# Optimization experiments

Hardware: AMD Instinct MI355X
Metric: run time of the kernel (lower is better)

## Reference

```python
import jax, jax.numpy as jnp
import numpy as np

NUM_HEADS = 16  # matches init_kwargs


def _linear(x, W, b):
    # torch nn.Linear: x @ W.T + b
    return jnp.matmul(x, W.T) + b


def setup_inputs() -> dict:
    key = jax.random.key(0)
    ks = jax.random.split(key, 5)
    B, S, Dm = 8, 2048, 1024
    scale = 0.02
    return {
        "q": jax.random.normal(ks[0], (B, S, Dm), dtype=jnp.float32),
        "k": jax.random.normal(ks[1], (B, S, Dm), dtype=jnp.float32),
        "v": jax.random.normal(ks[2], (B, S, Dm), dtype=jnp.float32),
        "W": jax.random.normal(ks[3], (Dm, Dm), dtype=jnp.float32) * scale,
        "b": jax.random.normal(ks[4], (Dm,), dtype=jnp.float32) * scale,
    }


def reference(q, k, v, W, b):
    B, S, Dm = q.shape
    H = NUM_HEADS
    D = Dm // H  # head_dim

    def proj(x):
        # linear -> view(B, S, H, D) -> transpose(2, 3): (B, S, D, H)
        # NOTE: original code transposes dims 2 and 3 (head_dim <-> heads),
        # NOT the usual (1, 2); we reproduce that exactly.
        y = _linear(x, W, b).reshape(B, S, H, D)
        return jnp.swapaxes(y, 2, 3)  # (B, S, D, H)

    qh, kh, vh = proj(q), proj(k), proj(v)

    # scores: (B, S, D, H) @ (B, S, H, D) -> (B, S, D, D), scaled by sqrt(head_dim)
    logits = jnp.einsum("bsdh,bseh->bsde", qh, kh) / jnp.sqrt(jnp.float32(D))
    attn = jax.nn.softmax(logits, axis=-1)
    out = jnp.einsum("bsde,bseh->bsdh", attn, vh)  # (B, S, D, H)

    # transpose(1, 2) -> (B, D, S, H), then view(B, -1, model_dim)
    concat = jnp.swapaxes(out, 1, 2).reshape(B, -1, Dm)  # (B, S, Dm)
    return _linear(concat, W, b)
```

## Files before the change

kernel.cpp:

```cpp
#include <hip/hip_runtime.h>
#include <hip/hip_fp16.h>
#include <math.h>

typedef _Float16 f16;
typedef _Float16 half8_t __attribute__((ext_vector_type(8)));
typedef _Float16 half2_t __attribute__((ext_vector_type(2)));
typedef __fp16   fp16x2  __attribute__((ext_vector_type(2)));
typedef float    float4_t __attribute__((ext_vector_type(4)));

__device__ f16 Wh[1024 * 1024];

__device__ __forceinline__ void gl_lds16(const void* g, void* l) {
    __builtin_amdgcn_global_load_lds(
        (const __attribute__((address_space(1))) void*)g,
        (__attribute__((address_space(3))) void*)l,
        16, 0, 0);
}

__device__ __forceinline__ half2_t pkrtz(float a, float b) {
    fp16x2 r = __builtin_amdgcn_cvt_pkrtz(a, b);
    return __builtin_bit_cast(half2_t, r);
}

__device__ __forceinline__ float fdot2(half2_t a, half2_t b, float c) {
    return __builtin_amdgcn_fdot2(__builtin_bit_cast(fp16x2, a),
                                  __builtin_bit_cast(fp16x2, b), c, false);
}

__device__ __forceinline__ half8_t cvt8(float4_t lo, float4_t hi) {
    half2_t p0 = pkrtz(lo[0], lo[1]);
    half2_t p1 = pkrtz(lo[2], lo[3]);
    half2_t p2 = pkrtz(hi[0], hi[1]);
    half2_t p3 = pkrtz(hi[2], hi[3]);
    half8_t r;
    r[0] = p0[0]; r[1] = p0[1]; r[2] = p1[0]; r[3] = p1[1];
    r[4] = p2[0]; r[5] = p2[1]; r[6] = p3[0]; r[7] = p3[1];
    return r;
}

__global__ __launch_bounds__(256) void convert_w_kernel(const float* __restrict__ W) {
    const int i = (blockIdx.x * 256 + threadIdx.x) * 8;
    const float4_t a = *(const float4_t*)(W + i);
    const float4_t b = *(const float4_t*)(W + i + 4);
    half8_t h;
#pragma unroll
    for (int t = 0; t < 4; ++t) h[t] = (f16)a[t];
#pragma unroll
    for (int t = 0; t < 4; ++t) h[4 + t] = (f16)b[t];
    *(half8_t*)(Wh + i) = h;
}

template <typename TA, typename TC>
__global__ __launch_bounds__(256) void gemm_kernel(
    const TA* __restrict__ A, const float* __restrict__ bias,
    TC* __restrict__ C)
{
    constexpr int K = 1024, N = 1024;
    constexpr bool AF32 = (sizeof(TA) == 4);
    __shared__ __align__(16) char smem[(AF32 ? 16384 : 8192) + 8192];
    float* Asf = (float*)smem;
    f16*   Ash = (f16*)smem;
    f16*   Bsh = (f16*)(smem + (AF32 ? 16384 : 8192));

    const int tid  = threadIdx.x;
    const int lane = tid & 63;
    const int wave = tid >> 6;
    const int wm = (wave >> 1) << 6;
    const int wn = (wave & 1) << 6;
    const int row0 = blockIdx.x * 128;
    const int col0 = blockIdx.y * 128;
    const int lrow = lane & 15;
    const int kq   = lane >> 4;

    float4_t acc[4][4];
#pragma unroll
    for (int i = 0; i < 4; ++i)
#pragma unroll
        for (int j = 0; j < 4; ++j)
            acc[i][j] = (float4_t){0.f, 0.f, 0.f, 0.f};

    for (int kt = 0; kt < K; kt += 32) {
#pragma unroll
        for (int it = 0; it < 2; ++it) {
            const int ch = tid + it * 256;
            const int r = ch >> 2, s = ch & 3;
            const f16* src = Wh + (size_t)(col0 + r) * K + kt + ((s ^ ((r >> 1) & 3)) << 3);
            gl_lds16(src, Bsh + ch * 8);
        }
        if constexpr (AF32) {
#pragma unroll
            for (int it = 0; it < 4; ++it) {
                const int ch = tid + it * 256;
                const int r = ch >> 3, s = ch & 7;
                const float* src = (const float*)A + (size_t)(row0 + r) * K + kt + ((s ^ (r & 7)) << 2);
                gl_lds16(src, Asf + ch * 4);
            }
        } else {
#pragma unroll
            for (int it = 0; it < 2; ++it) {
                const int ch = tid + it * 256;
                const int r = ch >> 2, s = ch & 3;
                const f16* src = (const f16*)A + (size_t)(row0 + r) * K + kt + ((s ^ ((r >> 1) & 3)) << 3);
                gl_lds16(src, Ash + ch * 8);
            }
        }
        __syncthreads();

        half8_t af[4], bf[4];
#pragma unroll
        for (int i = 0; i < 4; ++i) {
            const int m = wm + i * 16 + lrow;
            if constexpr (AF32) {
                const int c0 = kq * 2;
                const float4_t lo = *(const float4_t*)(Asf + m * 32 + ((c0 ^ (m & 7)) << 2));
                const float4_t hi = *(const float4_t*)(Asf + m * 32 + (((c0 + 1) ^ (m & 7)) << 2));
                af[i] = cvt8(lo, hi);
            } else {
                af[i] = *(const half8_t*)(Ash + m * 32 + ((kq ^ ((m >> 1) & 3)) << 3));
            }
        }
#pragma unroll
        for (int j = 0; j < 4; ++j) {
            const int n = wn + j * 16 + lrow;
            bf[j] = *(const half8_t*)(Bsh + n * 32 + ((kq ^ ((n >> 1) & 3)) << 3));
        }
#pragma unroll
        for (int i = 0; i < 4; ++i)
#pragma unroll
            for (int j = 0; j < 4; ++j)
                acc[i][j] = __builtin_amdgcn_mfma_f32_16x16x32_f16(af[i], bf[j], acc[i][j], 0, 0, 0);
        __syncthreads();
    }

    const int ccol  = lane & 15;
    const int rbase = (lane >> 4) << 2;
#pragma unroll
    for (int j = 0; j < 4; ++j) {
        const int gcol = col0 + wn + j * 16 + ccol;
        const float bv = bias[gcol];
#pragma unroll
        for (int i = 0; i < 4; ++i) {
#pragma unroll
            for (int r = 0; r < 4; ++r) {
                const int grow = row0 + wm + i * 16 + rbase + r;
                C[(size_t)grow * N + gcol] = (TC)(acc[i][j][r] + bv);
            }
        }
    }
}

__global__ __launch_bounds__(256) void attn_kernel(
    const f16* __restrict__ pq, const f16* __restrict__ pk,
    const f16* __restrict__ pv, f16* __restrict__ outp)
{
    __shared__ __align__(16) f16 Ks[4][64][24];
    __shared__ __align__(16) f16 Vs[4][16][72];
    const int lane = threadIdx.x & 63;
    const int wave = threadIdx.x >> 6;
    const int p = blockIdx.x * 4 + wave;
    const int b = p >> 11;
    const int s = p & 2047;
    const f16* qptr = pq + (size_t)p * 1024;
    const f16* kptr = pk + (size_t)p * 1024;
    const f16* vptr = pv + (size_t)p * 1024;

    {
        const int h  = lane >> 2;
        const int e0 = (lane & 3) << 4;
        const half8_t k0 = *(const half8_t*)(kptr + lane * 16);
        const half8_t k1 = *(const half8_t*)(kptr + lane * 16 + 8);
#pragma unroll
        for (int t = 0; t < 8; ++t) {
            Ks[wave][e0 + t][h]     = k0[t];
            Ks[wave][e0 + 8 + t][h] = k1[t];
        }
        const half8_t v0 = *(const half8_t*)(vptr + lane * 16);
        const half8_t v1 = *(const half8_t*)(vptr + lane * 16 + 8);
        *(half8_t*)&Vs[wave][h][e0]     = v0;
        *(half8_t*)&Vs[wave][h][e0 + 8] = v1;
    }
    half2_t qp2[8];
#pragma unroll
    for (int h2 = 0; h2 < 8; ++h2) {
        half2_t t;
        t[0] = qptr[(2 * h2) * 64 + lane];
        t[1] = qptr[(2 * h2 + 1) * 64 + lane];
        qp2[h2] = t;
    }
    __syncthreads();

    float a[64];
#pragma unroll
    for (int e = 0; e < 64; ++e) {
        const half8_t* kr = (const half8_t*)&Ks[wave][e][0];
        const half8_t ka = kr[0];
        const half8_t kb = kr[1];
        float acc = 0.f;
#pragma unroll
        for (int t = 0; t < 4; ++t) {
            half2_t k2a; k2a[0] = ka[2 * t]; k2a[1] = ka[2 * t + 1];
            half2_t k2b; k2b[0] = kb[2 * t]; k2b[1] = kb[2 * t + 1];
            acc = fdot2(qp2[t], k2a, acc);
            acc = fdot2(qp2[4 + t], k2b, acc);
        }
        a[e] = acc;
    }

    float m = a[0];
#pragma unroll
    for (int e = 1; e < 64; ++e) m = fmaxf(m, a[e]);
    float sum = 0.f;
#pragma unroll
    for (int e = 0; e < 64; ++e) {
        const float t = __expf((a[e] - m) * 0.125f);
        a[e] = t;
        sum += t;
    }
    const float inv = 1.f / sum;

    half2_t pk2[32];
#pragma unroll
    for (int e2 = 0; e2 < 32; ++e2)
        pk2[e2] = pkrtz(a[2 * e2], a[2 * e2 + 1]);

    float o[16];
#pragma unroll
    for (int h = 0; h < 16; ++h) {
        const half8_t* vr = (const half8_t*)&Vs[wave][h][0];
        float acc = 0.f;
#pragma unroll
        for (int q8 = 0; q8 < 8; ++q8) {
            const half8_t vv = vr[q8];
#pragma unroll
            for (int t = 0; t < 4; ++t) {
                half2_t v2; v2[0] = vv[2 * t]; v2[1] = vv[2 * t + 1];
                acc = fdot2(pk2[q8 * 4 + t], v2, acc);
            }
        }
        o[h] = acc;
    }

    half8_t o0, o1;
#pragma unroll
    for (int h = 0; h < 8; ++h) o0[h] = (f16)(o[h] * inv);
#pragma unroll
    for (int h = 0; h < 8; ++h) o1[h] = (f16)(o[8 + h] * inv);
    f16* dst = outp + ((size_t)(b * 64 + lane) * 2048 + s) * 16;
    *(half8_t*)dst       = o0;
    *(half8_t*)(dst + 8) = o1;
}

extern "C" void kernel_launch(void* const* d_in, const int* in_sizes, int n_in,
                              void* d_out, int out_size, void* d_ws, size_t ws_size,
                              hipStream_t stream)
{
    const float* q    = (const float*)d_in[0];
    const float* k    = (const float*)d_in[1];
    const float* v    = (const float*)d_in[2];
    const float* W    = (const float*)d_in[3];
    const float* bias = (const float*)d_in[4];
    float* out = (float*)d_out;

    const int M = 16384;
    const size_t elems = (size_t)M * 1024;

    f16* projq = (f16*)d_ws;
    f16* attn  = projq + elems;
    f16* projk = (f16*)d_out;
    f16* projv = projk + elems;

    convert_w_kernel<<<512, 256, 0, stream>>>(W);

    dim3 grid(M / 128, 1024 / 128);
    gemm_kernel<float, f16><<<grid, 256, 0, stream>>>(q, bias, projq);
    gemm_kernel<float, f16><<<grid, 256, 0, stream>>>(k, bias, projk);
    gemm_kernel<float, f16><<<grid, 256, 0, stream>>>(v, bias, projv);
    attn_kernel<<<M / 4, 256, 0, stream>>>(projq, projk, projv, attn);
    gemm_kernel<f16, float><<<grid, 256, 0, stream>>>(attn, bias, out);
}
```

Baseline: 480.8 us.

## Double GEMM K-tile to 64 and batch Q/K/V projections into one launch

The GEMM body moves into a device function whose K step per barrier grows from 32 to 64, with wider LDS tiles and adjusted XOR swizzles, which halves the number of sync/load rounds. The three projection GEMMs become one launch using grid z to pick q/k/v, removing launch gaps and tail effects. LDS use per block doubles (48KB for the f32 path), which may lower occupancy.

```diff
diff --git a/kernel.cpp b/kernel.cpp
--- a/kernel.cpp
+++ b/kernel.cpp
@@ -51,16 +51,16 @@
 }
 
 template <typename TA, typename TC>
-__global__ __launch_bounds__(256) void gemm_kernel(
+__device__ __forceinline__ void gemm_tile(
     const TA* __restrict__ A, const float* __restrict__ bias,
     TC* __restrict__ C)
 {
     constexpr int K = 1024, N = 1024;
     constexpr bool AF32 = (sizeof(TA) == 4);
-    __shared__ __align__(16) char smem[(AF32 ? 16384 : 8192) + 8192];
+    __shared__ __align__(16) char smem[(AF32 ? 32768 : 16384) + 16384];
     float* Asf = (float*)smem;
     f16*   Ash = (f16*)smem;
-    f16*   Bsh = (f16*)(smem + (AF32 ? 16384 : 8192));
+    f16*   Bsh = (f16*)(smem + (AF32 ? 32768 : 16384));
 
     const int tid  = threadIdx.x;
     const int lane = tid & 63;
@@ -79,56 +79,59 @@
         for (int j = 0; j < 4; ++j)
             acc[i][j] = (float4_t){0.f, 0.f, 0.f, 0.f};
 
-    for (int kt = 0; kt < K; kt += 32) {
-#pragma unroll
-        for (int it = 0; it < 2; ++it) {
+    for (int kt = 0; kt < K; kt += 64) {
+#pragma unroll
+        for (int it = 0; it < 4; ++it) {
             const int ch = tid + it * 256;
-            const int r = ch >> 2, s = ch & 3;
-            const f16* src = Wh + (size_t)(col0 + r) * K + kt + ((s ^ ((r >> 1) & 3)) << 3);
+            const int r = ch >> 3, s = ch & 7;
+            const f16* src = Wh + (size_t)(col0 + r) * K + kt + ((s ^ (r & 7)) << 3);
             gl_lds16(src, Bsh + ch * 8);
         }
         if constexpr (AF32) {
+#pragma unroll
+            for (int it = 0; it < 8; ++it) {
+                const int ch = tid + it * 256;
+                const int r = ch >> 4, s = ch & 15;
+                const float* src = (const float*)A + (size_t)(row0 + r) * K + kt + ((s ^ (r & 15)) << 2);
+                gl_lds16(src, Asf + ch * 4);
+            }
+        } else {
 #pragma unroll
             for (int it = 0; it < 4; ++it) {
                 const int ch = tid + it * 256;
                 const int r = ch >> 3, s = ch & 7;
-                const float* src = (const float*)A + (size_t)(row0 + r) * K + kt + ((s ^ (r & 7)) << 2);
-                gl_lds16(src, Asf + ch * 4);
-            }
-        } else {
-#pragma unroll
-            for (int it = 0; it < 2; ++it) {
-                const int ch = tid + it * 256;
-                const int r = ch >> 2, s = ch & 3;
-                const f16* src = (const f16*)A + (size_t)(row0 + r) * K + kt + ((s ^ ((r >> 1) & 3)) << 3);
+                const f16* src = (const f16*)A + (size_t)(row0 + r) * K + kt + ((s ^ (r & 7)) << 3);
                 gl_lds16(src, Ash + ch * 8);
             }
         }
         __syncthreads();
 
-        half8_t af[4], bf[4];
-#pragma unroll
-        for (int i = 0; i < 4; ++i) {
-            const int m = wm + i * 16 + lrow;
-            if constexpr (AF32) {
-                const int c0 = kq * 2;
-                const float4_t lo = *(const float4_t*)(Asf + m * 32 + ((c0 ^ (m & 7)) << 2));
-                const float4_t hi = *(const float4_t*)(Asf + m * 32 + (((c0 + 1) ^ (m & 7)) << 2));
-                af[i] = cvt8(lo, hi);
-            } else {
-                af[i] = *(const half8_t*)(Ash + m * 32 + ((kq ^ ((m >> 1) & 3)) << 3));
-            }
-        }
-#pragma unroll
-        for (int j = 0; j < 4; ++j) {
-            const int n = wn + j * 16 + lrow;
-            bf[j] = *(const half8_t*)(Bsh + n * 32 + ((kq ^ ((n >> 1) & 3)) << 3));
-        }
-#pragma unroll
-        for (int i = 0; i < 4; ++i)
-#pragma unroll
-            for (int j = 0; j < 4; ++j)
-                acc[i][j] = __builtin_amdgcn_mfma_f32_16x16x32_f16(af[i], bf[j], acc[i][j], 0, 0, 0);
+#pragma unroll
+        for (int ks = 0; ks < 2; ++ks) {
+            half8_t af[4], bf[4];
+#pragma unroll
+            for (int i = 0; i < 4; ++i) {
+                const int m = wm + i * 16 + lrow;
+                if constexpr (AF32) {
+                    const int c0 = ks * 8 + kq * 2;
+                    const float4_t lo = *(const float4_t*)(Asf + m * 64 + ((c0 ^ (m & 15)) << 2));
+                    const float4_t hi = *(const float4_t*)(Asf + m * 64 + (((c0 + 1) ^ (m & 15)) << 2));
+                    af[i] = cvt8(lo, hi);
+                } else {
+                    af[i] = *(const half8_t*)(Ash + m * 64 + (((ks * 4 + kq) ^ (m & 7)) << 3));
+                }
+            }
+#pragma unroll
+            for (int j = 0; j < 4; ++j) {
+                const int n = wn + j * 16 + lrow;
+                bf[j] = *(const half8_t*)(Bsh + n * 64 + (((ks * 4 + kq) ^ (n & 7)) << 3));
+            }
+#pragma unroll
+            for (int i = 0; i < 4; ++i)
+#pragma unroll
+                for (int j = 0; j < 4; ++j)
+                    acc[i][j] = __builtin_amdgcn_mfma_f32_16x16x32_f16(af[i], bf[j], acc[i][j], 0, 0, 0);
+        }
         __syncthreads();
     }
 
@@ -147,6 +150,25 @@
             }
         }
     }
+}
+
+template <typename TA, typename TC>
+__global__ __launch_bounds__(256) void gemm_kernel(
+    const TA* __restrict__ A, const float* __restrict__ bias,
+    TC* __restrict__ C)
+{
+    gemm_tile<TA, TC>(A, bias, C);
+}
+
+__global__ __launch_bounds__(256) void gemm_proj_kernel(
+    const float* __restrict__ q, const float* __restrict__ k,
+    const float* __restrict__ v, const float* __restrict__ bias,
+    f16* __restrict__ cq, f16* __restrict__ ck, f16* __restrict__ cv)
+{
+    const int z = blockIdx.z;
+    const float* A = (z == 0) ? q : (z == 1) ? k : v;
+    f16*         C = (z == 0) ? cq : (z == 1) ? ck : cv;
+    gemm_tile<float, f16>(A, bias, C);
 }
 
 __global__ __launch_bounds__(256) void attn_kernel(
@@ -271,10 +293,9 @@
 
     convert_w_kernel<<<512, 256, 0, stream>>>(W);
 
+    dim3 gridp(M / 128, 1024 / 128, 3);
+    gemm_proj_kernel<<<gridp, 256, 0, stream>>>(q, k, v, bias, projq, projk, projv);
+    attn_kernel<<<M / 4, 256, 0, stream>>>(projq, projk, projv, attn);
     dim3 grid(M / 128, 1024 / 128);
-    gemm_kernel<float, f16><<<grid, 256, 0, stream>>>(q, bias, projq);
-    gemm_kernel<float, f16><<<grid, 256, 0, stream>>>(k, bias, projk);
-    gemm_kernel<float, f16><<<grid, 256, 0, stream>>>(v, bias, projv);
-    attn_kernel<<<M / 4, 256, 0, stream>>>(projq, projk, projv, attn);
     gemm_kernel<f16, float><<<grid, 256, 0, stream>>>(attn, bias, out);
 }
```

Result: faster. 448.3 us (-6.8%).
